# Optimization experiments

Measured on AMD Instinct MI355X. Metric: run time of the kernel, lower is better.

## Reference

```python
import jax, jax.numpy as jnp
import numpy as np


def setup_inputs() -> dict:
    key = jax.random.key(0)
    ks = jax.random.split(key, 8)
    C = 256
    C8 = C // 8
    B, H, W = 8, 64, 64
    scale = 0.05
    return {
        "x": jax.random.normal(ks[0], (B, C, W, H), dtype=jnp.float32),
        "Wq": jax.random.normal(ks[1], (C8, C), dtype=jnp.float32) * scale,
        "bq": jax.random.normal(ks[2], (C8,), dtype=jnp.float32) * scale,
        "Wk": jax.random.normal(ks[3], (C8, C), dtype=jnp.float32) * scale,
        "bk": jax.random.normal(ks[4], (C8,), dtype=jnp.float32) * scale,
        "Wv": jax.random.normal(ks[5], (C, C), dtype=jnp.float32) * scale,
        "bv": jax.random.normal(ks[6], (C,), dtype=jnp.float32) * scale,
        "gamma": jax.random.normal(ks[7], (1,), dtype=jnp.float32),
    }


def reference(x, Wq, bq, Wk, bk, Wv, bv, gamma):
    B, C, W, H = x.shape
    N = W * H
    xf = x.reshape(B, C, N)  # flatten spatial dims: [B, C, N]
    # 1x1 convs == per-pixel channel matmuls
    q = jnp.einsum("oc,bcn->bno", Wq, xf) + bq  # [B, N, C/8]
    k = jnp.einsum("oc,bcn->bon", Wk, xf) + bk[None, :, None]  # [B, C/8, N]
    v = jnp.einsum("oc,bcn->bon", Wv, xf) + bv[None, :, None]  # [B, C, N]
    # unscaled QK^T softmax (dim=-1), as in the original
    attn = jax.nn.softmax(jnp.einsum("bno,bom->bnm", q, k), axis=-1)  # [B, N, N]
    # out[b,c,m] = sum_n v[b,c,n] * attn[b,m,n]
    out = jnp.einsum("bcn,bmn->bcm", v, attn).reshape(B, C, W, H)
    return gamma[0] * out + x
```

## Files before the change

kernel.cpp:

```cpp
#include <hip/hip_runtime.h>
#include <stdint.h>

#define B_ 8
#define C_ 256
#define N_ 4096

typedef __attribute__((ext_vector_type(8))) short short8;
typedef __attribute__((ext_vector_type(4))) float float4v;
typedef __attribute__((ext_vector_type(16))) float floatx16;

__device__ __forceinline__ uint16_t f2bfr(float f) {
  return (uint16_t)((__float_as_uint(f) + 0x8000u) >> 16);
}
__device__ __forceinline__ uint32_t pkbf(float lo, float hi) {
  return ((__float_as_uint(hi) + 0x8000u) & 0xffff0000u) |
         ((__float_as_uint(lo) + 0x8000u) >> 16);
}
__device__ __forceinline__ short8 ld8(const uint16_t* p) {
  union { ushort4 h[2]; short8 v; } u;
  u.h[0] = *reinterpret_cast<const ushort4*>(p);
  u.h[1] = *reinterpret_cast<const ushort4*>(p + 4);
  return u.v;
}

__global__ __launch_bounds__(256) void wconv_kernel(
    const float* __restrict__ Wq, const float* __restrict__ bq,
    const float* __restrict__ Wk, const float* __restrict__ bk,
    const float* __restrict__ Wv, const float* __restrict__ bv,
    uint16_t* __restrict__ Wc, float* __restrict__ bc)
{
  int tg = blockIdx.x * 256 + threadIdx.x;
  int idx = tg * 4;
  const float* src = (idx < 8192) ? (Wq + idx)
                   : (idx < 16384) ? (Wk + (idx - 8192))
                                   : (Wv + (idx - 16384));
  float4 wv = *reinterpret_cast<const float4*>(src);
  uint2 o;
  o.x = pkbf(wv.x, wv.y);
  o.y = pkbf(wv.z, wv.w);
  *reinterpret_cast<uint2*>(Wc + idx) = o;
  if (tg < 320) bc[tg] = (tg < 32) ? bq[tg] : (tg < 64) ? bk[tg - 32] : bv[tg - 64];
}

__global__ __launch_bounds__(512, 4) void qkv_mfma(
    const float* __restrict__ x, const uint16_t* __restrict__ Wc,
    const float* __restrict__ bc,
    uint16_t* __restrict__ Qw, uint16_t* __restrict__ Kw, uint16_t* __restrict__ Vw)
{
  __shared__ __align__(16) uint16_t xs[64][268];
  const int b = blockIdx.x & 7;
  const int tile = blockIdx.x >> 3;
  const int n0 = tile * 64;
  const int tid = threadIdx.x;
  const int nl = tid & 63, grp = tid >> 6;
  const int w = grp, l15 = tid & 15, q = (tid & 63) >> 4;
  const int nb = w & 3;

  const float* xb = x + (size_t)b * C_ * N_ + n0;
  #pragma unroll
  for (int it = 0; it < 16; ++it) {
    int c2 = it * 16 + grp * 2;
    float f0 = xb[(size_t)c2 * N_ + nl];
    float f1 = xb[(size_t)(c2 + 1) * N_ + nl];
    *reinterpret_cast<uint32_t*>(&xs[nl][c2]) = pkbf(f0, f1);
  }
  __syncthreads();

  float4v acc[10];
  #pragma unroll
  for (int i = 0; i < 10; ++i) acc[i] = (float4v){0.f, 0.f, 0.f, 0.f};

  const int ob0 = (w >> 2) * 10;
  #pragma unroll
  for (int h2 = 0; h2 < 2; ++h2) {
    short8 bx[4];
    #pragma unroll
    for (int kb = 0; kb < 4; ++kb)
      bx[kb] = ld8(&xs[nb * 16 + l15][h2 * 128 + kb * 32 + q * 8]);
    #pragma unroll
    for (int oi = 0; oi < 10; ++oi) {
      int ob = ob0 + oi;
      const uint16_t* wr = Wc + (size_t)(ob * 16 + l15) * 256 + h2 * 128 + q * 8;
      short8 aw[4];
      #pragma unroll
      for (int kb = 0; kb < 4; ++kb)
        aw[kb] = *reinterpret_cast<const short8*>(wr + kb * 32);
      #pragma unroll
      for (int kb = 0; kb < 4; ++kb)
        acc[oi] = __builtin_amdgcn_mfma_f32_16x16x32_bf16(aw[kb], bx[kb], acc[oi], 0, 0, 0);
    }
  }

  __syncthreads();
  uint16_t (*qs)[72] = reinterpret_cast<uint16_t(*)[72]>(&xs[0][0]);
  if (w < 4) {
    #pragma unroll
    for (int oi = 0; oi < 4; ++oi) {
      float4v a = acc[oi];
      const float* bb = bc + oi * 16 + q * 4;
      uint2 pk2;
      pk2.x = pkbf(a.x + bb[0], a.y + bb[1]);
      pk2.y = pkbf(a.z + bb[2], a.w + bb[3]);
      *reinterpret_cast<uint2*>(&qs[nb * 16 + l15][oi * 16 + q * 4]) = pk2;
    }
  }
  __syncthreads();
  if (tid < 256) {
    int n = tid >> 2, sub = tid & 3;
    const uint16_t* row = qs[n];
    uint4 d0 = *reinterpret_cast<const uint4*>(&row[sub * 16]);
    uint4 d1 = *reinterpret_cast<const uint4*>(&row[sub * 16 + 8]);
    size_t nn = (size_t)b * N_ + n0 + n;
    if (sub < 2) {
      uint4* dst = reinterpret_cast<uint4*>(Qw + nn * 32 + sub * 16);
      dst[0] = d0; dst[1] = d1;
    } else {
      uint4* dst = reinterpret_cast<uint4*>(Kw + nn * 32 + (sub - 2) * 16);
      dst[0] = d0; dst[1] = d1;
    }
  }
  const size_t blk = ((size_t)b * 64 + tile) * 4;
  const int half = l15 >> 3, j = l15 & 7;
  #pragma unroll
  for (int oi = 0; oi < 10; ++oi) {
    int ob = ob0 + oi;
    if (ob < 4) continue;
    float4v a = acc[oi];
    const float* bb = bc + ob * 16 + q * 4;
    int cb = ob * 16 - 64 + q * 4;
    size_t vaddr = (blk + (cb >> 6)) * 4096
                 + (size_t)(nb * 1024 + ((cb >> 5) & 1) * 512 + half * 256
                            + (cb & 31) * 8 + j);
    Vw[vaddr     ] = f2bfr(a.x + bb[0]);
    Vw[vaddr +  8] = f2bfr(a.y + bb[1]);
    Vw[vaddr + 16] = f2bfr(a.z + bb[2]);
    Vw[vaddr + 24] = f2bfr(a.w + bb[3]);
  }
}

__global__ __launch_bounds__(512, 4) void attn_mfma(
    const uint16_t* __restrict__ Qw, const uint16_t* __restrict__ Kw,
    const uint16_t* __restrict__ Vw, const float* __restrict__ x,
    const float* __restrict__ gamma, float* __restrict__ out)
{
  __shared__ __align__(16) union Smem {
    uint16_t Ps[2][64 * 76];
    float Os[128 * 69];
  } sm;
  __shared__ float Ls[64];

  const int b = blockIdx.x & 7;
  const int m0 = (blockIdx.x >> 3) * 64;
  const int tid = threadIdx.x;
  const int w = tid >> 6, lane = tid & 63;
  const int l15 = lane & 15, q = lane >> 4;
  const int l31 = lane & 31, half = lane >> 5;
  const int nb = w & 3, mbp = (w >> 2) * 2;

  const uint16_t* Kb = Kw + (size_t)b * N_ * 32 + (size_t)(nb * 16 + l15) * 32 + q * 8;
  const short8 qf0 = *reinterpret_cast<const short8*>(
      Qw + ((size_t)b * N_ + m0 + (mbp    ) * 16 + l15) * 32 + q * 8);
  const short8 qf1 = *reinterpret_cast<const short8*>(
      Qw + ((size_t)b * N_ + m0 + (mbp + 1) * 16 + l15) * 32 + q * 8);
  const uint16_t* Vb = Vw + ((size_t)b * 256 + (w >> 1)) * 4096
                     + (w & 1) * 512 + half * 256 + l31 * 8;

  floatx16 O[2];
  #pragma unroll
  for (int i = 0; i < 16; ++i) { O[0][i] = 0.f; O[1][i] = 0.f; }
  float rs0 = 0.f, rs1 = 0.f;
  const float4v zero4 = (float4v){0.f, 0.f, 0.f, 0.f};
  if (tid < 64) Ls[tid] = 0.f;

  {
    short8 kf = *reinterpret_cast<const short8*>(Kb);
    float4v s0 = __builtin_amdgcn_mfma_f32_16x16x32_bf16(kf, qf0, zero4, 0, 0, 0);
    float4v s1 = __builtin_amdgcn_mfma_f32_16x16x32_bf16(kf, qf1, zero4, 0, 0, 0);
    float p0 = __expf(s0.x), p1 = __expf(s0.y), p2 = __expf(s0.z), p3 = __expf(s0.w);
    rs0 += (p0 + p1) + (p2 + p3);
    uint2 pw; pw.x = pkbf(p0, p1); pw.y = pkbf(p2, p3);
    *reinterpret_cast<uint2*>(&sm.Ps[0][((mbp)*16 + l15) * 76 + nb * 16 + q * 4]) = pw;
    float r0 = __expf(s1.x), r1 = __expf(s1.y), r2 = __expf(s1.z), r3 = __expf(s1.w);
    rs1 += (r0 + r1) + (r2 + r3);
    uint2 rw; rw.x = pkbf(r0, r1); rw.y = pkbf(r2, r3);
    *reinterpret_cast<uint2*>(&sm.Ps[0][((mbp + 1)*16 + l15) * 76 + nb * 16 + q * 4]) = rw;
  }
  __syncthreads();

  for (int t = 0; t < 64; ++t) {
    const int buf = t & 1;

    short8 kf;
    if (t < 63)
      kf = *reinterpret_cast<const short8*>(Kb + (size_t)(t + 1) * 64 * 32);
    short8 vf[4];
    const uint16_t* vt = Vb + (size_t)t * 16384;
    #pragma unroll
    for (int ks = 0; ks < 4; ++ks)
      vf[ks] = *reinterpret_cast<const short8*>(vt + ks * 1024);

    if (t < 63) {
      float4v s0 = __builtin_amdgcn_mfma_f32_16x16x32_bf16(kf, qf0, zero4, 0, 0, 0);
      float4v s1 = __builtin_amdgcn_mfma_f32_16x16x32_bf16(kf, qf1, zero4, 0, 0, 0);
      float p0 = __expf(s0.x), p1 = __expf(s0.y), p2 = __expf(s0.z), p3 = __expf(s0.w);
      rs0 += (p0 + p1) + (p2 + p3);
      uint2 pw; pw.x = pkbf(p0, p1); pw.y = pkbf(p2, p3);
      *reinterpret_cast<uint2*>(&sm.Ps[buf ^ 1][((mbp)*16 + l15) * 76 + nb * 16 + q * 4]) = pw;
      float r0 = __expf(s1.x), r1 = __expf(s1.y), r2 = __expf(s1.z), r3 = __expf(s1.w);
      rs1 += (r0 + r1) + (r2 + r3);
      uint2 rw; rw.x = pkbf(r0, r1); rw.y = pkbf(r2, r3);
      *reinterpret_cast<uint2*>(&sm.Ps[buf ^ 1][((mbp + 1)*16 + l15) * 76 + nb * 16 + q * 4]) = rw;
    }

    #pragma unroll
    for (int ks = 0; ks < 4; ++ks) {
      short8 pa0 = ld8(&sm.Ps[buf][(l31     ) * 76 + ks * 16 + half * 8]);
      short8 pa1 = ld8(&sm.Ps[buf][(32 + l31) * 76 + ks * 16 + half * 8]);
      O[0] = __builtin_amdgcn_mfma_f32_32x32x16_bf16(pa0, vf[ks], O[0], 0, 0, 0);
      O[1] = __builtin_amdgcn_mfma_f32_32x32x16_bf16(pa1, vf[ks], O[1], 0, 0, 0);
    }
    __syncthreads();
  }

  rs0 += __shfl_xor(rs0, 16); rs0 += __shfl_xor(rs0, 32);
  rs1 += __shfl_xor(rs1, 16); rs1 += __shfl_xor(rs1, 32);
  if (q == 0) {
    atomicAdd(&Ls[(mbp    ) * 16 + l15], rs0);
    atomicAdd(&Ls[(mbp + 1) * 16 + l15], rs1);
  }
  __syncthreads();
  if (tid < 64) Ls[tid] = gamma[0] / Ls[tid];
  __syncthreads();

  #pragma unroll
  for (int chunk = 0; chunk < 2; ++chunk) {
    if ((w >> 2) == chunk) {
      int cl = (w & 3) * 32 + l31;
      #pragma unroll
      for (int h = 0; h < 2; ++h)
        #pragma unroll
        for (int reg = 0; reg < 16; ++reg) {
          int m = h * 32 + (reg & 3) + 8 * (reg >> 2) + 4 * half;
          sm.Os[cl * 69 + m] = O[h][reg] * Ls[m];
        }
    }
    __syncthreads();
    {
      int cl = tid >> 2, msub = tid & 3;
      int c = chunk * 128 + cl;
      size_t idx = ((size_t)b * C_ + c) * N_ + m0 + msub * 16;
      const float* os = &sm.Os[cl * 69 + msub * 16];
      #pragma unroll
      for (int i = 0; i < 4; ++i) {
        float4 xv = *reinterpret_cast<const float4*>(x + idx + i * 4);
        float4 ov;
        ov.x = os[i * 4 + 0] + xv.x;
        ov.y = os[i * 4 + 1] + xv.y;
        ov.z = os[i * 4 + 2] + xv.z;
        ov.w = os[i * 4 + 3] + xv.w;
        *reinterpret_cast<float4*>(out + idx + i * 4) = ov;
      }
    }
    __syncthreads();
  }
}

extern "C" void kernel_launch(void* const* d_in, const int* in_sizes, int n_in,
                              void* d_out, int out_size, void* d_ws, size_t ws_size,
                              hipStream_t stream) {
  const float* x     = (const float*)d_in[0];
  const float* Wq    = (const float*)d_in[1];
  const float* bq    = (const float*)d_in[2];
  const float* Wk    = (const float*)d_in[3];
  const float* bk    = (const float*)d_in[4];
  const float* Wv    = (const float*)d_in[5];
  const float* bv    = (const float*)d_in[6];
  const float* gamma = (const float*)d_in[7];
  float* out = (float*)d_out;

  uint16_t* Qw = (uint16_t*)d_ws;
  uint16_t* Kw = Qw + (size_t)B_ * N_ * 32;
  uint16_t* Vw = Kw + (size_t)B_ * N_ * 32;
  uint16_t* Wc = Vw + (size_t)B_ * C_ * N_;
  float*    bc = (float*)(Wc + 320 * 256);

  wconv_kernel<<<80, 256, 0, stream>>>(Wq, bq, Wk, bk, Wv, bv, Wc, bc);
  qkv_mfma<<<512, 512, 0, stream>>>(x, Wc, bc, Qw, Kw, Vw);
  attn_mfma<<<512, 512, 0, stream>>>(Qw, Kw, Vw, x, gamma, out);
}
```

Before: 231.5 us.

## Unroll attention loop by two with register double-buffered K/V prefetch

Restructures the main attention loop into a manually unrolled pair of phases that ping-pong between two register sets for V and K fragments, prefetching one tile ahead so global loads overlap the current tile's MFMAs. The first PV step's LDS loads are hoisted before the S-phase exp/pack work so MFMA and exp can interleave. This increases register pressure and code size, which may lower occupancy.

New measurement: 231.1 us. About the same (-0.2%).

```diff
diff --git a/kernel.cpp b/kernel.cpp
--- a/kernel.cpp
+++ b/kernel.cpp
@@ -172,54 +172,74 @@
   const float4v zero4 = (float4v){0.f, 0.f, 0.f, 0.f};
   if (tid < 64) Ls[tid] = 0.f;
 
-  {
-    short8 kf = *reinterpret_cast<const short8*>(Kb);
-    float4v s0 = __builtin_amdgcn_mfma_f32_16x16x32_bf16(kf, qf0, zero4, 0, 0, 0);
-    float4v s1 = __builtin_amdgcn_mfma_f32_16x16x32_bf16(kf, qf1, zero4, 0, 0, 0);
+  auto s_phase = [&](short8 kfrag, uint16_t* __restrict__ dst) {
+    float4v s0 = __builtin_amdgcn_mfma_f32_16x16x32_bf16(kfrag, qf0, zero4, 0, 0, 0);
+    float4v s1 = __builtin_amdgcn_mfma_f32_16x16x32_bf16(kfrag, qf1, zero4, 0, 0, 0);
     float p0 = __expf(s0.x), p1 = __expf(s0.y), p2 = __expf(s0.z), p3 = __expf(s0.w);
     rs0 += (p0 + p1) + (p2 + p3);
     uint2 pw; pw.x = pkbf(p0, p1); pw.y = pkbf(p2, p3);
-    *reinterpret_cast<uint2*>(&sm.Ps[0][((mbp)*16 + l15) * 76 + nb * 16 + q * 4]) = pw;
+    *reinterpret_cast<uint2*>(&dst[((mbp)*16 + l15) * 76 + nb * 16 + q * 4]) = pw;
     float r0 = __expf(s1.x), r1 = __expf(s1.y), r2 = __expf(s1.z), r3 = __expf(s1.w);
     rs1 += (r0 + r1) + (r2 + r3);
     uint2 rw; rw.x = pkbf(r0, r1); rw.y = pkbf(r2, r3);
-    *reinterpret_cast<uint2*>(&sm.Ps[0][((mbp + 1)*16 + l15) * 76 + nb * 16 + q * 4]) = rw;
-  }
-  __syncthreads();
-
-  for (int t = 0; t < 64; ++t) {
-    const int buf = t & 1;
-
-    short8 kf;
-    if (t < 63)
-      kf = *reinterpret_cast<const short8*>(Kb + (size_t)(t + 1) * 64 * 32);
-    short8 vf[4];
-    const uint16_t* vt = Vb + (size_t)t * 16384;
+    *reinterpret_cast<uint2*>(&dst[((mbp + 1)*16 + l15) * 76 + nb * 16 + q * 4]) = rw;
+  };
+  auto pv_tail = [&](const uint16_t* __restrict__ src, const short8* vf) {
     #pragma unroll
-    for (int ks = 0; ks < 4; ++ks)
-      vf[ks] = *reinterpret_cast<const short8*>(vt + ks * 1024);
-
-    if (t < 63) {
-      float4v s0 = __builtin_amdgcn_mfma_f32_16x16x32_bf16(kf, qf0, zero4, 0, 0, 0);
-      float4v s1 = __builtin_amdgcn_mfma_f32_16x16x32_bf16(kf, qf1, zero4, 0, 0, 0);
-      float p0 = __expf(s0.x), p1 = __expf(s0.y), p2 = __expf(s0.z), p3 = __expf(s0.w);
-      rs0 += (p0 + p1) + (p2 + p3);
-      uint2 pw; pw.x = pkbf(p0, p1); pw.y = pkbf(p2, p3);
-      *reinterpret_cast<uint2*>(&sm.Ps[buf ^ 1][((mbp)*16 + l15) * 76 + nb * 16 + q * 4]) = pw;
-      float r0 = __expf(s1.x), r1 = __expf(s1.y), r2 = __expf(s1.z), r3 = __expf(s1.w);
-      rs1 += (r0 + r1) + (r2 + r3);
-      uint2 rw; rw.x = pkbf(r0, r1); rw.y = pkbf(r2, r3);
-      *reinterpret_cast<uint2*>(&sm.Ps[buf ^ 1][((mbp + 1)*16 + l15) * 76 + nb * 16 + q * 4]) = rw;
-    }
-
-    #pragma unroll
-    for (int ks = 0; ks < 4; ++ks) {
-      short8 pa0 = ld8(&sm.Ps[buf][(l31     ) * 76 + ks * 16 + half * 8]);
-      short8 pa1 = ld8(&sm.Ps[buf][(32 + l31) * 76 + ks * 16 + half * 8]);
+    for (int ks = 1; ks < 4; ++ks) {
+      short8 pa0 = ld8(&src[(l31     ) * 76 + ks * 16 + half * 8]);
+      short8 pa1 = ld8(&src[(32 + l31) * 76 + ks * 16 + half * 8]);
       O[0] = __builtin_amdgcn_mfma_f32_32x32x16_bf16(pa0, vf[ks], O[0], 0, 0, 0);
       O[1] = __builtin_amdgcn_mfma_f32_32x32x16_bf16(pa1, vf[ks], O[1], 0, 0, 0);
     }
-    __syncthreads();
+  };
+
+  short8 vA[4], vB[4], kA, kB;
+  #pragma unroll
+  for (int ks = 0; ks < 4; ++ks)
+    vA[ks] = *reinterpret_cast<const short8*>(Vb + ks * 1024);
+  kA = *reinterpret_cast<const short8*>(Kb + (size_t)1 * 2048);
+  {
+    short8 k0 = *reinterpret_cast<const short8*>(Kb);
+    s_phase(k0, &sm.Ps[0][0]);
+  }
+  __syncthreads();
+
+  const uint16_t* vload = Vb + (size_t)16384;
+  const uint16_t* kload = Kb + (size_t)2 * 2048;
+
+  #pragma unroll 1
+  for (int u = 0; u < 32; ++u) {
+    {
+      #pragma unroll
+      for (int ks = 0; ks < 4; ++ks)
+        vB[ks] = *reinterpret_cast<const short8*>(vload + ks * 1024);
+      if (u < 31) kB = *reinterpret_cast<const short8*>(kload);
+      vload += 16384; kload += 2048;
+      short8 h0 = ld8(&sm.Ps[0][(l31     ) * 76 + half * 8]);
+      short8 h1 = ld8(&sm.Ps[0][(32 + l31) * 76 + half * 8]);
+      s_phase(kA, &sm.Ps[1][0]);
+      O[0] = __builtin_amdgcn_mfma_f32_32x32x16_bf16(h0, vA[0], O[0], 0, 0, 0);
+      O[1] = __builtin_amdgcn_mfma_f32_32x32x16_bf16(h1, vA[0], O[1], 0, 0, 0);
+      pv_tail(&sm.Ps[0][0], vA);
+      __syncthreads();
+    }
+    {
+      if (u < 31) {
+        #pragma unroll
+        for (int ks = 0; ks < 4; ++ks)
+          vA[ks] = *reinterpret_cast<const short8*>(vload + ks * 1024);
+        kA = *reinterpret_cast<const short8*>(kload);
+      }
+      vload += 16384; kload += 2048;
+      short8 h0 = ld8(&sm.Ps[1][(l31     ) * 76 + half * 8]);
+      short8 h1 = ld8(&sm.Ps[1][(32 + l31) * 76 + half * 8]);
+      if (u < 31) s_phase(kB, &sm.Ps[0][0]);
+      O[0] = __builtin_amdgcn_mfma_f32_32x32x16_bf16(h0, vB[0], O[0], 0, 0, 0);
+      O[1] = __builtin_amdgcn_mfma_f32_32x32x16_bf16(h1, vB[0], O[1], 0, 0, 0);
+      pv_tail(&sm.Ps[1][0], vB);
+      __syncthreads();
+    }
   }
 
   rs0 += __shfl_xor(rs0, 16); rs0 += __shfl_xor(rs0, 32);
```
